# Performance work log

Measured on AMD Instinct MI355X. Metric: run time of the kernel, lower is better.

## Reference

```python
import jax, jax.numpy as jnp
import numpy as np

N = 50000      # nodes
E = 800000     # edges
B = 512        # graphs in batch
DRNL = 64      # drnl_dim (feature_dim = 0)
H = 256        # hidden


def setup_inputs() -> dict:
    key = jax.random.key(0)
    ks = jax.random.split(key, 12)
    x = jax.random.normal(ks[0], (N, DRNL), jnp.float32)
    edge_index = jax.random.randint(ks[1], (2, E), 0, N)
    batch_vec = jnp.sort(jax.random.randint(ks[2], (N,), 0, B))
    u_idx = jax.random.randint(ks[3], (B,), 0, N)
    v_idx = jax.random.randint(ks[4], (B,), 0, N)

    def glorot(k, shp):
        scale = jnp.sqrt(2.0 / (shp[0] + shp[1]))
        return (jax.random.normal(k, shp, jnp.float32) * scale).astype(jnp.float32)

    W0 = glorot(ks[5], (DRNL, H)); b0 = jnp.zeros((H,), jnp.float32)
    W1 = glorot(ks[6], (H, H));    b1 = jnp.zeros((H,), jnp.float32)
    W2 = glorot(ks[7], (H, H));    b2 = jnp.zeros((H,), jnp.float32)
    Wm1 = glorot(ks[8], (3 * H, H)); bm1 = jnp.zeros((H,), jnp.float32)
    Wm2 = glorot(ks[9], (H, 1));     bm2 = jnp.zeros((1,), jnp.float32)
    return dict(x=x, edge_index=edge_index, batch_vec=batch_vec,
                u_idx=u_idx, v_idx=v_idx,
                W0=W0, b0=b0, W1=W1, b1=b1, W2=W2, b2=b2,
                Wm1=Wm1, bm1=bm1, Wm2=Wm2, bm2=bm2)


def _gcn_encode(x, src, dst, Ws, bs):
    # Standard GCN: h' = D^-1/2 (A + I) D^-1/2 h W + b, ReLU between layers.
    n = x.shape[0]
    loop = jnp.arange(n)
    src2 = jnp.concatenate([src, loop])  # add self-loops
    dst2 = jnp.concatenate([dst, loop])
    deg = jax.ops.segment_sum(jnp.ones_like(dst2, x.dtype), dst2, num_segments=n)
    dis = jax.lax.rsqrt(jnp.maximum(deg, 1.0))          # D^-1/2
    norm = dis[src2] * dis[dst2]                         # per-edge norm [E+N]

    h = x
    for i, (W, b) in enumerate(zip(Ws, bs)):
        msg = h[src2] * norm[:, None]                    # gather + scale
        agg = jax.ops.segment_sum(msg, dst2, num_segments=n)
        h = agg @ W + b
        if i < len(Ws) - 1:
            h = jax.nn.relu(h)
    return h


def reference(x, edge_index, batch_vec, u_idx, v_idx,
              W0, b0, W1, b1, W2, b2, Wm1, bm1, Wm2, bm2):
    src, dst = edge_index[0], edge_index[1]
    h = _gcn_encode(x, src, dst, (W0, W1, W2), (b0, b1, b2))   # [N, H]

    # global_mean_pool over batch_vec -> [B, H]
    cnt = jax.ops.segment_sum(jnp.ones((h.shape[0],), h.dtype), batch_vec,
                              num_segments=B)
    g = jax.ops.segment_sum(h, batch_vec, num_segments=B) / \
        jnp.maximum(cnt, 1.0)[:, None]

    # concat [g, h[u], h[v]] -> MLP -> [B] logits
    z = jnp.concatenate([g, h[u_idx], h[v_idx]], axis=1)       # [B, 3H]
    z = jax.nn.relu(z @ Wm1 + bm1)
    return (z @ Wm2 + bm2).squeeze(-1)
```

## Files before the change

kernel.cpp:

```cpp
#include <hip/hip_runtime.h>
#include <hip/hip_bf16.h>
#include <stdint.h>

#ifndef DRNL
#define DRNL 64
#define HDIM 256
#endif

#define CHUNK 4096
#define BCAP 3072
#define SCAP 1536

typedef __attribute__((ext_vector_type(4))) float f32x4;
typedef __attribute__((ext_vector_type(8))) _Float16 f16x8;

__device__ __forceinline__ void async16(void* lds, const void* g) {
    __builtin_amdgcn_global_load_lds(
        (const __attribute__((address_space(1))) void*)g,
        (__attribute__((address_space(3))) void*)(char*)lds, 16, 0, 0);
}

__device__ __forceinline__ int imin(int a, int b) { return a < b ? a : b; }

__global__ __launch_bounds__(256) void k_misc(
    const int* __restrict__ batch,
    const float* __restrict__ x,
    const float* __restrict__ W0, const float* __restrict__ W1,
    const float* __restrict__ W2,
    int* __restrict__ gstart,
    _Float16* __restrict__ x16,
    _Float16* __restrict__ W0t, _Float16* __restrict__ W1t,
    _Float16* __restrict__ W2t,
    const int* __restrict__ dst, int* __restrict__ ghist,
    int E, int P, int SH, int NBUCK,
    int N, int B) {
    const int tid = threadIdx.x;

    if (blockIdx.x < P) {
        __shared__ int h[512];
        int p = blockIdx.x;
        for (int i = tid; i < NBUCK; i += 256) h[i] = 0;
        __syncthreads();
        int e0 = p * CHUNK, e1 = imin(e0 + CHUNK, E);
        for (int e = e0 + tid; e < e1; e += 256)
            atomicAdd(&h[dst[e] >> SH], 1);
        __syncthreads();
        for (int b = tid; b < NBUCK; b += 256)
            ghist[(size_t)b * P + p] = h[b];
        return;
    }

    const int bid  = blockIdx.x - P;
    const int gsz  = (gridDim.x - P) * 256;
    const int gid0 = bid * 256 + tid;

    for (int i = gid0; i < (DRNL + 2 * HDIM) * 256; i += gsz) {
        int b = i >> 8, c = i & 255;
        const float* W; _Float16* T; int k, K;
        if (b < DRNL)            { W = W0; T = W0t; k = b;              K = DRNL; }
        else if (b < DRNL + 256) { W = W1; T = W1t; k = b - DRNL;       K = HDIM; }
        else                     { W = W2; T = W2t; k = b - DRNL - 256; K = HDIM; }
        int KT = K >> 5;
        int cg = c >> 6, ct = (c >> 4) & 3, cl = c & 15;
        int kt = k >> 5, qq = (k >> 3) & 3, j = k & 7;
        int lane = (qq << 4) | cl;
        T[(((size_t)(cg * KT + kt) * 4 + ct) * 64 + lane) * 8 + j] =
            (_Float16)W[(size_t)k * 256 + c];
    }

    {
        const float4* x4 = (const float4*)x;
        f16x8* xv = (f16x8*)x16;
        int tot = N * DRNL / 8;
        for (int i = gid0; i < tot; i += gsz) {
            float4 a = x4[2 * i], b2 = x4[2 * i + 1];
            f16x8 o;
            o[0] = (_Float16)a.x;  o[1] = (_Float16)a.y;
            o[2] = (_Float16)a.z;  o[3] = (_Float16)a.w;
            o[4] = (_Float16)b2.x; o[5] = (_Float16)b2.y;
            o[6] = (_Float16)b2.z; o[7] = (_Float16)b2.w;
            xv[i] = o;
        }
    }

    for (int i = gid0; i <= N; i += gsz) {
        if (i == 0) {
            int b0 = batch[0];
            for (int b = 0; b <= b0; ++b) gstart[b] = 0;
        } else if (i == N) {
            int bl = batch[N - 1];
            for (int b = bl + 1; b <= B; ++b) gstart[b] = N;
        } else {
            int bp = batch[i - 1], bc = batch[i];
            if (bc != bp)
                for (int b = bp + 1; b <= bc; ++b) gstart[b] = i;
        }
    }
}

__global__ __launch_bounds__(256) void k_gbase(int* __restrict__ ghist,
                                               int* __restrict__ btot, int P) {
    __shared__ int s[256];
    int b = blockIdx.x, tid = threadIdx.x;
    int* row = ghist + (size_t)b * P;
    int carry = 0;
    for (int base = 0; base < P; base += 256) {
        int idx = base + tid;
        int v = (idx < P) ? row[idx] : 0;
        s[tid] = v;
        __syncthreads();
        for (int o = 1; o < 256; o <<= 1) {
            int t = (tid >= o) ? s[tid - o] : 0;
            __syncthreads();
            s[tid] += t;
            __syncthreads();
        }
        if (idx < P) row[idx] = carry + s[tid] - v;
        carry += s[255];
        __syncthreads();
    }
    if (tid == 0) btot[b] = carry;
}

__global__ __launch_bounds__(256) void k_btscan(const int* __restrict__ btot,
                                                int* __restrict__ bbase,
                                                int* __restrict__ rowptr,
                                                int NBUCK, int N, int E) {
    __shared__ int s[256];
    int tid = threadIdx.x;
    int carry = 0;
    for (int base = 0; base < NBUCK; base += 256) {
        int idx = base + tid;
        int v = (idx < NBUCK) ? btot[idx] : 0;
        s[tid] = v;
        __syncthreads();
        for (int o = 1; o < 256; o <<= 1) {
            int t = (tid >= o) ? s[tid - o] : 0;
            __syncthreads();
            s[tid] += t;
            __syncthreads();
        }
        if (idx < NBUCK) bbase[idx] = carry + s[tid] - v;
        carry += s[255];
        __syncthreads();
    }
    if (tid == 0) { bbase[NBUCK] = E; rowptr[N] = E; }
}

__global__ __launch_bounds__(256) void k_scatter(const int* __restrict__ src,
                                                 const int* __restrict__ dst,
                                                 const int* __restrict__ ghist,
                                                 const int* __restrict__ bbase,
                                                 int* __restrict__ tmp,
                                                 int E, int P, int SH, int NBUCK) {
    __shared__ int base[512];
    int p = blockIdx.x, tid = threadIdx.x;
    for (int b = tid; b < NBUCK; b += 256)
        base[b] = bbase[b] + ghist[(size_t)b * P + p];
    __syncthreads();
    int e0 = p * CHUNK, e1 = imin(e0 + CHUNK, E);
    int msk = (1 << SH) - 1;
    for (int e = e0 + tid; e < e1; e += 256) {
        int d = dst[e];
        int r = atomicAdd(&base[d >> SH], 1);
        tmp[r] = (src[e] << SH) | (d & msk);
    }
}

__global__ __launch_bounds__(256) void k_bsort(const int* __restrict__ tmp,
                                               const int* __restrict__ bbase,
                                               int* __restrict__ col,
                                               int* __restrict__ rowptr,
                                               float* __restrict__ dis,
                                               _Float16* __restrict__ x16,
                                               int SH, int N) {
    __shared__ int cnt[512];
    __shared__ int off[512];
    __shared__ int sscan[256];
    __shared__ int eL[BCAP];
    __shared__ unsigned short rnk[BCAP];
    __shared__ int sL[BCAP];
    int b = blockIdx.x, tid = threadIdx.x;
    int nodes = 1 << SH, node0 = b << SH, msk = nodes - 1;
    int lo = bbase[b], hi = bbase[b + 1], m = hi - lo;
    bool fast = (m <= BCAP);

    for (int i = tid; i < nodes; i += 256) cnt[i] = 0;
    __syncthreads();
    if (fast) {
        for (int i = tid; i < m; i += 256) {
            int v = tmp[lo + i];
            eL[i] = v;
            rnk[i] = (unsigned short)atomicAdd(&cnt[v & msk], 1);
        }
    } else {
        for (int i = tid; i < m; i += 256)
            atomicAdd(&cnt[tmp[lo + i] & msk], 1);
    }
    __syncthreads();
    int carry = 0;
    for (int base = 0; base < nodes; base += 256) {
        int idx = base + tid;
        int v = (idx < nodes) ? cnt[idx] : 0;
        sscan[tid] = v;
        __syncthreads();
        for (int o = 1; o < 256; o <<= 1) {
            int t = (tid >= o) ? sscan[tid - o] : 0;
            __syncthreads();
            sscan[tid] += t;
            __syncthreads();
        }
        if (idx < nodes) off[idx] = carry + sscan[tid] - v;
        carry += sscan[255];
        __syncthreads();
    }
    for (int i = tid; i < nodes; i += 256) {
        int node = node0 + i;
        if (node < N) {
            rowptr[node] = lo + off[i];
            dis[node]    = rsqrtf((float)cnt[i] + 1.f);
        }
    }
    int rlim = imin(nodes, N - node0);
    for (int u = tid; u < rlim * 8; u += 256) {
        int r = u >> 3, c = u & 7;
        float d = rsqrtf((float)cnt[r] + 1.f);
        f16x8* xv = (f16x8*)(x16 + (size_t)(node0 + r) * 64);
        f16x8 v = xv[c];
        f16x8 o;
#pragma unroll
        for (int k = 0; k < 8; ++k) o[k] = (_Float16)((float)v[k] * d);
        xv[c] = o;
    }
    __syncthreads();
    if (fast) {
        for (int i = tid; i < m; i += 256) {
            int v = eL[i];
            sL[off[v & msk] + rnk[i]] = v >> SH;
        }
        __syncthreads();
        for (int i = tid; i < m; i += 256) col[lo + i] = sL[i];
    } else {
        for (int i = tid; i < nodes; i += 256) cnt[i] = 0;
        __syncthreads();
        for (int i = tid; i < m; i += 256) {
            int v = tmp[lo + i];
            int d = v & msk;
            int r = atomicAdd(&cnt[d], 1);
            col[lo + off[d] + r] = v >> SH;
        }
    }
}

template <int FBLK>
__global__ __launch_bounds__(256) void k_agg(const _Float16* __restrict__ hs,
                                             const float* __restrict__ dis,
                                             const int* __restrict__ rowptr,
                                             const int* __restrict__ col,
                                             _Float16* __restrict__ A16, int N) {
    __shared__ int scol[SCAP];
    int node_wg, f;
    if constexpr (FBLK == 4) {
        int wg = blockIdx.x;
        int xcd = wg & 7;
        f = xcd >> 1;
        int half = xcd & 1;
        int NH = gridDim.x >> 3;
        node_wg = half * NH + (wg >> 3);
    } else {
        node_wg = blockIdx.x;
        f = 0;
    }
    const int n0 = imin(node_wg * 32, N);
    const int n1 = imin(node_wg * 32 + 32, N);
    const int e_lo = rowptr[n0];
    const int cnt = rowptr[n1] - e_lo;
    const bool useLds = (cnt <= SCAP);
    if (useLds)
        for (int i = threadIdx.x; i < cnt; i += 256) scol[i] = col[e_lo + i];
    __syncthreads();

    int lane = threadIdx.x & 63;
    int wv = threadIdx.x >> 6;
    int oct = lane >> 3;
    int fl = lane & 7;
    int gw = node_wg * 32 + wv * 8 + oct;
    bool valid = gw < N;
    int gwc = valid ? gw : N - 1;
    const size_t boff = (size_t)f * ((size_t)N * 64);
    const f16x8* hv = (const f16x8*)(hs + boff);
    float acc[8];
#pragma unroll
    for (int k = 0; k < 8; ++k) acc[k] = 0.f;

    int e0 = rowptr[gwc];
    int e1 = valid ? rowptr[gwc + 1] : e0;

    if (useLds) {
        int j  = e0 - e_lo;
        int eN = valid ? e1 - e_lo : j;
        while (__any(j < eN)) {
            bool a0 = j < eN, a1 = j + 1 < eN, a2 = j + 2 < eN, a3 = j + 3 < eN;
            int s0 = scol[a0 ? j : 0];
            int s1 = scol[a1 ? j + 1 : 0];
            int s2 = scol[a2 ? j + 2 : 0];
            int s3 = scol[a3 ? j + 3 : 0];
            float m0 = a0 ? 1.f : 0.f, m1 = a1 ? 1.f : 0.f;
            float m2 = a2 ? 1.f : 0.f, m3 = a3 ? 1.f : 0.f;
            f16x8 v0 = hv[(size_t)s0 * 8 + fl];
            f16x8 v1 = hv[(size_t)s1 * 8 + fl];
            f16x8 v2 = hv[(size_t)s2 * 8 + fl];
            f16x8 v3 = hv[(size_t)s3 * 8 + fl];
#pragma unroll
            for (int k = 0; k < 8; ++k) acc[k] += m0 * (float)v0[k];
#pragma unroll
            for (int k = 0; k < 8; ++k) acc[k] += m1 * (float)v1[k];
#pragma unroll
            for (int k = 0; k < 8; ++k) acc[k] += m2 * (float)v2[k];
#pragma unroll
            for (int k = 0; k < 8; ++k) acc[k] += m3 * (float)v3[k];
            j += 4;
        }
    } else {
        int j = e0;
        while (__any(j < e1)) {
            bool a0 = j < e1, a1 = j + 1 < e1, a2 = j + 2 < e1, a3 = j + 3 < e1;
            int s0 = col[a0 ? j : 0];
            int s1 = col[a1 ? j + 1 : 0];
            int s2 = col[a2 ? j + 2 : 0];
            int s3 = col[a3 ? j + 3 : 0];
            float m0 = a0 ? 1.f : 0.f, m1 = a1 ? 1.f : 0.f;
            float m2 = a2 ? 1.f : 0.f, m3 = a3 ? 1.f : 0.f;
            f16x8 v0 = hv[(size_t)s0 * 8 + fl];
            f16x8 v1 = hv[(size_t)s1 * 8 + fl];
            f16x8 v2 = hv[(size_t)s2 * 8 + fl];
            f16x8 v3 = hv[(size_t)s3 * 8 + fl];
#pragma unroll
            for (int k = 0; k < 8; ++k) acc[k] += m0 * (float)v0[k];
#pragma unroll
            for (int k = 0; k < 8; ++k) acc[k] += m1 * (float)v1[k];
#pragma unroll
            for (int k = 0; k < 8; ++k) acc[k] += m2 * (float)v2[k];
#pragma unroll
            for (int k = 0; k < 8; ++k) acc[k] += m3 * (float)v3[k];
            j += 4;
        }
    }

    float dn = dis[gwc];
    f16x8 hsv = hv[(size_t)gwc * 8 + fl];
    f16x8 o;
#pragma unroll
    for (int k = 0; k < 8; ++k)
        o[k] = (_Float16)((acc[k] + (float)hsv[k]) * dn);
    if (valid)
        __builtin_nontemporal_store(
            o, (f16x8*)(A16 + boff + (size_t)gw * 64 + fl * 8));
}

template <int K, int OUT_RELU, int SCALE>
__global__ __launch_bounds__(256, 1) void k_wgemm(const _Float16* __restrict__ A,
                                                  const _Float16* __restrict__ Wf,
                                                  const float* __restrict__ bias,
                                                  const float* __restrict__ dis,
                                                  _Float16* __restrict__ outh, int n) {
    constexpr int KT  = K / 32;
    constexpr int NFB = K / 64;
    constexpr int NI  = NFB * 2;
    constexpr int STG = NFB * 1024;
    __shared__ _Float16 sAll[4 * (STG + 1024)];

    const int tid  = threadIdx.x;
    const int lane = tid & 63;
    const int wv   = tid >> 6;
    const int c15  = lane & 15;
    const int q    = lane >> 4;
    const int row0 = blockIdx.x * 64;
    const size_t bstride = (size_t)n * 64;
    _Float16* sbuf = sAll + wv * (STG + 1024);
    _Float16* sO   = sbuf + STG;
    _Float16* ob   = outh + (size_t)wv * bstride;

    f16x8 wf[4][KT];
    const _Float16* wp = Wf + ((size_t)wv * KT * 4 * 64 + lane) * 8;
#pragma unroll
    for (int kt = 0; kt < KT; ++kt)
#pragma unroll
        for (int ct = 0; ct < 4; ++ct)
            wf[ct][kt] = *(const f16x8*)(wp + (size_t)((kt * 4 + ct) * 64) * 8);

    float bvl = bias[(wv << 6) + lane];
    float bv[4];
#pragma unroll
    for (int ct = 0; ct < 4; ++ct) bv[ct] = __shfl(bvl, (ct << 4) + c15);

    float dsv[4][4];
    if (SCALE) {
        float dvl = dis[imin(row0 + lane, n - 1)];
#pragma unroll
        for (int st = 0; st < 4; ++st)
#pragma unroll
            for (int r = 0; r < 4; ++r)
                dsv[st][r] = __shfl(dvl, (st << 4) + (q << 2) + r);
    }

#pragma unroll
    for (int st = 0; st < 4; ++st) {
        const int r0 = row0 + (st << 4);
#pragma unroll
        for (int i = 0; i < NI; ++i) {
            int s   = (i << 6) + lane;
            int fb  = s >> 7;
            int row = (s >> 3) & 15;
            int ch  = (s & 7) ^ (row & 7);
            int gr  = imin(r0 + row, n - 1);
            async16(sbuf + (size_t)s * 8,
                    A + (size_t)fb * bstride + (size_t)gr * 64 + ch * 8);
        }
        asm volatile("s_waitcnt vmcnt(0)" ::: "memory");
        __builtin_amdgcn_sched_barrier(0);

        f16x8 af[KT];
#pragma unroll
        for (int kt = 0; kt < KT; ++kt) {
            int off = (kt >> 1) * 1024 + c15 * 64 +
                      ((((kt & 1) * 4 + q) ^ (c15 & 7)) * 8);
            af[kt] = *(const f16x8*)(sbuf + off);
        }

        f32x4 acc[4];
#pragma unroll
        for (int ct = 0; ct < 4; ++ct) acc[ct] = (f32x4)0.f;
#pragma unroll
        for (int kt = 0; kt < KT; ++kt)
#pragma unroll
            for (int ct = 0; ct < 4; ++ct)
                acc[ct] = __builtin_amdgcn_mfma_f32_16x16x32_f16(
                    af[kt], wf[ct][kt], acc[ct], 0, 0, 0);

#pragma unroll
        for (int ct = 0; ct < 4; ++ct) {
#pragma unroll
            for (int r = 0; r < 4; ++r) {
                float v = acc[ct][r] + bv[ct];
                if (OUT_RELU) v = fmaxf(v, 0.f);
                if (SCALE) v *= dsv[st][r];
                int row = (q << 2) + r;
                int colx = (ct << 4) + c15;
                int sw = (((colx >> 3) ^ (row & 7)) << 3) | (colx & 7);
                sO[row * 64 + sw] = (_Float16)v;
            }
        }
#pragma unroll
        for (int ps = 0; ps < 2; ++ps) {
            int u = (ps << 6) + lane;
            int rr = u >> 3, ch2 = u & 7;
            f16x8 vv = *(const f16x8*)(sO + rr * 64 + ((ch2 ^ (rr & 7)) << 3));
            if (r0 + rr < n)
                *(f16x8*)(ob + (size_t)(r0 + rr) * 64 + ch2 * 8) = vv;
        }
    }
}

__global__ __launch_bounds__(256) void k_head(const _Float16* __restrict__ h,
                                              const int* __restrict__ gstart,
                                              const int* __restrict__ u,
                                              const int* __restrict__ v,
                                              const float* __restrict__ Wm1,
                                              const float* __restrict__ bm1,
                                              const float* __restrict__ Wm2,
                                              const float* __restrict__ bm2,
                                              float* __restrict__ out, int N) {
    int b = blockIdx.x;
    int t = threadIdx.x;
    __shared__ float z[3 * HDIM];
    __shared__ float red[4];
    const _Float16* hb = h + (size_t)(t >> 6) * ((size_t)N * 64) + (t & 63);
    int s = gstart[b], e = gstart[b + 1];
    float pa = 0.f;
    int i = s;
    for (; i + 3 < e; i += 4) {
        float a0 = (float)hb[(size_t)i * 64];
        float a1 = (float)hb[(size_t)(i + 1) * 64];
        float a2 = (float)hb[(size_t)(i + 2) * 64];
        float a3 = (float)hb[(size_t)(i + 3) * 64];
        pa += (a0 + a1) + (a2 + a3);
    }
    for (; i < e; ++i) pa += (float)hb[(size_t)i * 64];
    z[t]            = pa / fmaxf((float)(e - s), 1.f);
    z[HDIM + t]     = (float)hb[(size_t)u[b] * 64];
    z[2 * HDIM + t] = (float)hb[(size_t)v[b] * 64];
    __syncthreads();
    float acc[8];
#pragma unroll
    for (int k = 0; k < 8; ++k) acc[k] = 0.f;
    for (int k = 0; k < 3 * HDIM; k += 8) {
#pragma unroll
        for (int jj = 0; jj < 8; ++jj)
            acc[jj] = fmaf(z[k + jj], Wm1[(size_t)(k + jj) * HDIM + t], acc[jj]);
    }
    float sum = (((acc[0] + acc[1]) + (acc[2] + acc[3])) +
                 ((acc[4] + acc[5]) + (acc[6] + acc[7]))) + bm1[t];
    float hid = fmaxf(sum, 0.f);
    float p = hid * Wm2[t];
    for (int off = 32; off; off >>= 1) p += __shfl_down(p, off);
    if ((t & 63) == 0) red[t >> 6] = p;
    __syncthreads();
    if (t == 0) out[b] = red[0] + red[1] + red[2] + red[3] + bm2[0];
}

extern "C" void kernel_launch(void* const* d_in, const int* in_sizes, int n_in,
                              void* d_out, int out_size, void* d_ws, size_t ws_size,
                              hipStream_t stream) {
    const float* x    = (const float*)d_in[0];
    const int*   ei   = (const int*)d_in[1];
    const int*   batc = (const int*)d_in[2];
    const int*   uidx = (const int*)d_in[3];
    const int*   vidx = (const int*)d_in[4];
    const float* W0   = (const float*)d_in[5];
    const float* b0   = (const float*)d_in[6];
    const float* W1   = (const float*)d_in[7];
    const float* b1   = (const float*)d_in[8];
    const float* W2   = (const float*)d_in[9];
    const float* b2   = (const float*)d_in[10];
    const float* Wm1  = (const float*)d_in[11];
    const float* bm1  = (const float*)d_in[12];
    const float* Wm2  = (const float*)d_in[13];
    const float* bm2  = (const float*)d_in[14];
    float* out = (float*)d_out;

    const int N = in_sizes[0] / DRNL;
    const int E = in_sizes[1] / 2;
    const int B = in_sizes[3];
    const int* src = ei;
    const int* dst = ei + E;

    int SH = 7;
    while (((N + (1 << SH) - 1) >> SH) > 512) ++SH;
    const int NBUCK = (N + (1 << SH) - 1) >> SH;
    const int P = (E + CHUNK - 1) / CHUNK;

    char* w = (char*)d_ws;
    size_t off = 0;
    auto carve = [&](size_t bytes) {
        void* p = w + off;
        off = (off + bytes + 255) & ~(size_t)255;
        return p;
    };
    int*       rowptr = (int*)carve((size_t)(N + 1) * 4);
    int*       colA   = (int*)carve((size_t)E * 4);
    float*     dis    = (float*)carve((size_t)N * 4);
    int*       gstart = (int*)carve((size_t)(B + 1) * 4);
    _Float16*  A16    = (_Float16*)carve((size_t)N * HDIM * 2);
    _Float16*  h16    = (_Float16*)carve((size_t)N * HDIM * 2);
    _Float16*  x16    = (_Float16*)carve((size_t)N * DRNL * 2);
    _Float16*  W0t    = (_Float16*)carve((size_t)DRNL * HDIM * 2);
    _Float16*  W1t    = (_Float16*)carve((size_t)HDIM * HDIM * 2);
    _Float16*  W2t    = (_Float16*)carve((size_t)HDIM * HDIM * 2);
    int*       ghist  = (int*)carve((size_t)NBUCK * P * 4);
    int*       btot   = (int*)carve(512 * 4);
    int*       bbase  = (int*)carve(513 * 4);
    int*       tmpE   = (int*)carve((size_t)E * 4);
    (void)ws_size;

    k_misc<<<P + 1024, 256, 0, stream>>>(batc, x, W0, W1, W2, gstart,
                                         x16, W0t, W1t, W2t,
                                         dst, ghist, E, P, SH, NBUCK, N, B);
    k_gbase<<<NBUCK, 256, 0, stream>>>(ghist, btot, P);
    k_btscan<<<1, 256, 0, stream>>>(btot, bbase, rowptr, NBUCK, N, E);
    k_scatter<<<P, 256, 0, stream>>>(src, dst, ghist, bbase, tmpE, E, P, SH, NBUCK);
    k_bsort<<<NBUCK, 256, 0, stream>>>(tmpE, bbase, colA, rowptr, dis, x16, SH, N);

    int gemmb = (N + 63) / 64;
    int NB = (N + 31) / 32;
    int NH = (NB + 1) / 2;
    int aggb4 = 8 * NH;

    k_agg<1><<<NB, 256, 0, stream>>>(x16, dis, rowptr, colA, A16, N);
    k_wgemm<DRNL, 1, 1><<<gemmb, 256, 0, stream>>>(A16, W0t, b0, dis, h16, N);
    k_agg<4><<<aggb4, 256, 0, stream>>>(h16, dis, rowptr, colA, A16, N);
    k_wgemm<HDIM, 1, 1><<<gemmb, 256, 0, stream>>>(A16, W1t, b1, dis, h16, N);
    k_agg<4><<<aggb4, 256, 0, stream>>>(h16, dis, rowptr, colA, A16, N);
    k_wgemm<HDIM, 0, 0><<<gemmb, 256, 0, stream>>>(A16, W2t, b2, dis, h16, N);

    k_head<<<B, 256, 0, stream>>>(h16, gstart, uidx, vidx, Wm1, bm1, Wm2, bm2, out, N);
}
```

Baseline: 286.3 us.

## Degree-sort nodes within buckets for aggregation and double-buffer GEMM A staging

The bucket sort now builds a per-bucket permutation that orders nodes by in-degree (capped at 63). The aggregation kernels walk nodes through this permutation, so the 8 nodes sharing a wave have similar edge counts, which reduces divergence and idle lanes. To make that work, each aggregation block stages the whole bucket's column list into LDS, and the LDS capacity is doubled to hold it. Separately, the weight GEMM now double-buffers its A-tile async loads so the next 16-row stage is fetched while the current one runs on MFMA. The costs are more LDS per block and an extra indirection for every node lookup; the larger stage also makes the LDS fallback path more likely.

```diff
diff --git a/kernel.cpp b/kernel.cpp
--- a/kernel.cpp
+++ b/kernel.cpp
@@ -9,7 +9,7 @@
 
 #define CHUNK 4096
 #define BCAP 3072
-#define SCAP 1536
+#define SCAP 3072
 
 typedef __attribute__((ext_vector_type(4))) float f32x4;
 typedef __attribute__((ext_vector_type(8))) _Float16 f16x8;
@@ -173,10 +173,13 @@
                                                int* __restrict__ rowptr,
                                                float* __restrict__ dis,
                                                _Float16* __restrict__ x16,
+                                               int* __restrict__ perm,
                                                int SH, int N) {
     __shared__ int cnt[512];
     __shared__ int off[512];
     __shared__ int sscan[256];
+    __shared__ int dh[64];
+    __shared__ int dbs[64];
     __shared__ int eL[BCAP];
     __shared__ unsigned short rnk[BCAP];
     __shared__ int sL[BCAP];
@@ -186,6 +189,7 @@
     bool fast = (m <= BCAP);
 
     for (int i = tid; i < nodes; i += 256) cnt[i] = 0;
+    for (int i = tid; i < 64; i += 256) dh[i] = 0;
     __syncthreads();
     if (fast) {
         for (int i = tid; i < m; i += 256) {
@@ -214,6 +218,7 @@
         carry += sscan[255];
         __syncthreads();
     }
+    int rlim = imin(nodes, N - node0);
     for (int i = tid; i < nodes; i += 256) {
         int node = node0 + i;
         if (node < N) {
@@ -221,7 +226,21 @@
             dis[node]    = rsqrtf((float)cnt[i] + 1.f);
         }
     }
-    int rlim = imin(nodes, N - node0);
+    for (int i = tid; i < rlim; i += 256)
+        atomicAdd(&dh[imin(cnt[i], 63)], 1);
+    __syncthreads();
+    if (tid == 0) {
+        int c = 0;
+        for (int d = 0; d < 64; ++d) { int t = dh[d]; dbs[d] = c; c += t; }
+    }
+    __syncthreads();
+    for (int i = tid; i < 64; i += 256) dh[i] = 0;
+    __syncthreads();
+    for (int i = tid; i < rlim; i += 256) {
+        int d = imin(cnt[i], 63);
+        int r = dbs[d] + atomicAdd(&dh[d], 1);
+        perm[node0 + r] = node0 + i;
+    }
     for (int u = tid; u < rlim * 8; u += 256) {
         int r = u >> 3, c = u & 7;
         float d = rsqrtf((float)cnt[r] + 1.f);
@@ -257,7 +276,9 @@
                                              const float* __restrict__ dis,
                                              const int* __restrict__ rowptr,
                                              const int* __restrict__ col,
-                                             _Float16* __restrict__ A16, int N) {
+                                             const int* __restrict__ perm,
+                                             _Float16* __restrict__ A16,
+                                             int N, int SH) {
     __shared__ int scol[SCAP];
     int node_wg, f;
     if constexpr (FBLK == 4) {
@@ -271,30 +292,32 @@
         node_wg = blockIdx.x;
         f = 0;
     }
-    const int n0 = imin(node_wg * 32, N);
-    const int n1 = imin(node_wg * 32 + 32, N);
-    const int e_lo = rowptr[n0];
-    const int cnt = rowptr[n1] - e_lo;
-    const bool useLds = (cnt <= SCAP);
+    if (node_wg * 32 >= N) return;
+    const int buck = (node_wg * 32) >> SH;
+    const int b_lo = buck << SH;
+    const int b_hi = imin(b_lo + (1 << SH), N);
+    const int e_lo = rowptr[b_lo];
+    const int cntE = rowptr[b_hi] - e_lo;
+    const bool useLds = (cntE <= SCAP);
     if (useLds)
-        for (int i = threadIdx.x; i < cnt; i += 256) scol[i] = col[e_lo + i];
+        for (int i = threadIdx.x; i < cntE; i += 256) scol[i] = col[e_lo + i];
     __syncthreads();
 
     int lane = threadIdx.x & 63;
     int wv = threadIdx.x >> 6;
     int oct = lane >> 3;
     int fl = lane & 7;
-    int gw = node_wg * 32 + wv * 8 + oct;
-    bool valid = gw < N;
-    int gwc = valid ? gw : N - 1;
+    int slot = node_wg * 32 + wv * 8 + oct;
+    bool valid = slot < N;
+    int gw = valid ? perm[slot] : 0;
     const size_t boff = (size_t)f * ((size_t)N * 64);
     const f16x8* hv = (const f16x8*)(hs + boff);
     float acc[8];
 #pragma unroll
     for (int k = 0; k < 8; ++k) acc[k] = 0.f;
 
-    int e0 = rowptr[gwc];
-    int e1 = valid ? rowptr[gwc + 1] : e0;
+    int e0 = rowptr[gw];
+    int e1 = valid ? rowptr[gw + 1] : e0;
 
     if (useLds) {
         int j  = e0 - e_lo;
@@ -347,8 +370,8 @@
         }
     }
 
-    float dn = dis[gwc];
-    f16x8 hsv = hv[(size_t)gwc * 8 + fl];
+    float dn = dis[gw];
+    f16x8 hsv = hv[(size_t)gw * 8 + fl];
     f16x8 o;
 #pragma unroll
     for (int k = 0; k < 8; ++k)
@@ -368,7 +391,7 @@
     constexpr int NFB = K / 64;
     constexpr int NI  = NFB * 2;
     constexpr int STG = NFB * 1024;
-    __shared__ _Float16 sAll[4 * (STG + 1024)];
+    __shared__ _Float16 sAll[4 * (2 * STG + 1024)];
 
     const int tid  = threadIdx.x;
     const int lane = tid & 63;
@@ -377,35 +400,12 @@
     const int q    = lane >> 4;
     const int row0 = blockIdx.x * 64;
     const size_t bstride = (size_t)n * 64;
-    _Float16* sbuf = sAll + wv * (STG + 1024);
-    _Float16* sO   = sbuf + STG;
-    _Float16* ob   = outh + (size_t)wv * bstride;
-
-    f16x8 wf[4][KT];
-    const _Float16* wp = Wf + ((size_t)wv * KT * 4 * 64 + lane) * 8;
-#pragma unroll
-    for (int kt = 0; kt < KT; ++kt)
-#pragma unroll
-        for (int ct = 0; ct < 4; ++ct)
-            wf[ct][kt] = *(const f16x8*)(wp + (size_t)((kt * 4 + ct) * 64) * 8);
-
-    float bvl = bias[(wv << 6) + lane];
-    float bv[4];
-#pragma unroll
-    for (int ct = 0; ct < 4; ++ct) bv[ct] = __shfl(bvl, (ct << 4) + c15);
-
-    float dsv[4][4];
-    if (SCALE) {
-        float dvl = dis[imin(row0 + lane, n - 1)];
-#pragma unroll
-        for (int st = 0; st < 4; ++st)
-#pragma unroll
-            for (int r = 0; r < 4; ++r)
-                dsv[st][r] = __shfl(dvl, (st << 4) + (q << 2) + r);
-    }
-
-#pragma unroll
-    for (int st = 0; st < 4; ++st) {
+    _Float16* sbufA = sAll + wv * (2 * STG + 1024);
+    _Float16* sbufB = sbufA + STG;
+    _Float16* sO    = sbufA + 2 * STG;
+    _Float16* ob    = outh + (size_t)wv * bstride;
+
+    auto stage = [&](_Float16* dstp, int st) {
         const int r0 = row0 + (st << 4);
 #pragma unroll
         for (int i = 0; i < NI; ++i) {
@@ -414,18 +414,56 @@
             int row = (s >> 3) & 15;
             int ch  = (s & 7) ^ (row & 7);
             int gr  = imin(r0 + row, n - 1);
-            async16(sbuf + (size_t)s * 8,
+            async16(dstp + (size_t)s * 8,
                     A + (size_t)fb * bstride + (size_t)gr * 64 + ch * 8);
         }
-        asm volatile("s_waitcnt vmcnt(0)" ::: "memory");
+    };
+
+    stage(sbufA, 0);
+
+    f16x8 wf[4][KT];
+    const _Float16* wp = Wf + ((size_t)wv * KT * 4 * 64 + lane) * 8;
+#pragma unroll
+    for (int kt = 0; kt < KT; ++kt)
+#pragma unroll
+        for (int ct = 0; ct < 4; ++ct)
+            wf[ct][kt] = *(const f16x8*)(wp + (size_t)((kt * 4 + ct) * 64) * 8);
+
+    float bvl = bias[(wv << 6) + lane];
+    float bv[4];
+#pragma unroll
+    for (int ct = 0; ct < 4; ++ct) bv[ct] = __shfl(bvl, (ct << 4) + c15);
+
+    float dsv[4][4];
+    if (SCALE) {
+        float dvl = dis[imin(row0 + lane, n - 1)];
+#pragma unroll
+        for (int st = 0; st < 4; ++st)
+#pragma unroll
+            for (int r = 0; r < 4; ++r)
+                dsv[st][r] = __shfl(dvl, (st << 4) + (q << 2) + r);
+    }
+
+#pragma unroll
+    for (int st = 0; st < 4; ++st) {
+        if (st < 3) stage((st & 1) ? sbufA : sbufB, st + 1);
+        if (st < 3) {
+            if constexpr (NI == 8)
+                asm volatile("s_waitcnt vmcnt(8)" ::: "memory");
+            else
+                asm volatile("s_waitcnt vmcnt(2)" ::: "memory");
+        } else {
+            asm volatile("s_waitcnt vmcnt(2)" ::: "memory");
+        }
         __builtin_amdgcn_sched_barrier(0);
 
+        const _Float16* buf = (st & 1) ? sbufB : sbufA;
         f16x8 af[KT];
 #pragma unroll
         for (int kt = 0; kt < KT; ++kt) {
             int off = (kt >> 1) * 1024 + c15 * 64 +
                       ((((kt & 1) * 4 + q) ^ (c15 & 7)) * 8);
-            af[kt] = *(const f16x8*)(sbuf + off);
+            af[kt] = *(const f16x8*)(buf + off);
         }
 
         f32x4 acc[4];
@@ -438,6 +476,7 @@
                 acc[ct] = __builtin_amdgcn_mfma_f32_16x16x32_f16(
                     af[kt], wf[ct][kt], acc[ct], 0, 0, 0);
 
+        const int r0 = row0 + (st << 4);
 #pragma unroll
         for (int ct = 0; ct < 4; ++ct) {
 #pragma unroll
@@ -551,6 +590,7 @@
     int*       colA   = (int*)carve((size_t)E * 4);
     float*     dis    = (float*)carve((size_t)N * 4);
     int*       gstart = (int*)carve((size_t)(B + 1) * 4);
+    int*       perm   = (int*)carve((size_t)N * 4);
     _Float16*  A16    = (_Float16*)carve((size_t)N * HDIM * 2);
     _Float16*  h16    = (_Float16*)carve((size_t)N * HDIM * 2);
     _Float16*  x16    = (_Float16*)carve((size_t)N * DRNL * 2);
@@ -569,18 +609,19 @@
     k_gbase<<<NBUCK, 256, 0, stream>>>(ghist, btot, P);
     k_btscan<<<1, 256, 0, stream>>>(btot, bbase, rowptr, NBUCK, N, E);
     k_scatter<<<P, 256, 0, stream>>>(src, dst, ghist, bbase, tmpE, E, P, SH, NBUCK);
-    k_bsort<<<NBUCK, 256, 0, stream>>>(tmpE, bbase, colA, rowptr, dis, x16, SH, N);
+    k_bsort<<<NBUCK, 256, 0, stream>>>(tmpE, bbase, colA, rowptr, dis, x16,
+                                       perm, SH, N);
 
     int gemmb = (N + 63) / 64;
     int NB = (N + 31) / 32;
     int NH = (NB + 1) / 2;
     int aggb4 = 8 * NH;
 
-    k_agg<1><<<NB, 256, 0, stream>>>(x16, dis, rowptr, colA, A16, N);
+    k_agg<1><<<NB, 256, 0, stream>>>(x16, dis, rowptr, colA, perm, A16, N, SH);
     k_wgemm<DRNL, 1, 1><<<gemmb, 256, 0, stream>>>(A16, W0t, b0, dis, h16, N);
-    k_agg<4><<<aggb4, 256, 0, stream>>>(h16, dis, rowptr, colA, A16, N);
+    k_agg<4><<<aggb4, 256, 0, stream>>>(h16, dis, rowptr, colA, perm, A16, N, SH);
     k_wgemm<HDIM, 1, 1><<<gemmb, 256, 0, stream>>>(A16, W1t, b1, dis, h16, N);
-    k_agg<4><<<aggb4, 256, 0, stream>>>(h16, dis, rowptr, colA, A16, N);
+    k_agg<4><<<aggb4, 256, 0, stream>>>(h16, dis, rowptr, colA, perm, A16, N, SH);
     k_wgemm<HDIM, 0, 0><<<gemmb, 256, 0, stream>>>(A16, W2t, b2, dis, h16, N);
 
     k_head<<<B, 256, 0, stream>>>(h16, gstart, uidx, vidx, Wm1, bm1, Wm2, bm2, out, N);
```

Result: slower. 296.4 us (+3.5%).

## Fuse layer-0 aggregation with its weight GEMM into one kernel

Applied to the files above, without the earlier changes.

Replaces the separate layer-0 aggregation kernel and the K=64 GEMM kernel with one fused kernel. Each workgroup aggregates 64 rows of neighbour features into LDS, then multiplies them by W0 using MFMA, with weights held in registers, and applies bias, ReLU and degree scaling. The A16 intermediate no longer makes a round trip through global memory and one launch is removed. In exchange, each workgroup runs the gather and the GEMM serially, uses fewer workgroups than the old 32-node aggregation grid, and needs more LDS.

```diff
diff --git a/kernel.cpp b/kernel.cpp
--- a/kernel.cpp
+++ b/kernel.cpp
@@ -10,6 +10,7 @@
 #define CHUNK 4096
 #define BCAP 3072
 #define SCAP 1536
+#define SCAP0 2048
 
 typedef __attribute__((ext_vector_type(4))) float f32x4;
 typedef __attribute__((ext_vector_type(8))) _Float16 f16x8;
@@ -252,25 +253,185 @@
     }
 }
 
-template <int FBLK>
-__global__ __launch_bounds__(256) void k_agg(const _Float16* __restrict__ hs,
-                                             const float* __restrict__ dis,
-                                             const int* __restrict__ rowptr,
-                                             const int* __restrict__ col,
-                                             _Float16* __restrict__ A16, int N) {
+__global__ __launch_bounds__(256) void k_l0(
+    const _Float16* __restrict__ hs, const float* __restrict__ dis,
+    const int* __restrict__ rowptr, const int* __restrict__ col,
+    const _Float16* __restrict__ Wf, const float* __restrict__ bias,
+    _Float16* __restrict__ outh, int n) {
+    constexpr int KT = 2;
+    __shared__ _Float16 sA[64 * 64];
+    __shared__ int scol[SCAP0];
+    __shared__ _Float16 sOut[4 * 16 * 64];
+
+    const int tid  = threadIdx.x;
+    const int lane = tid & 63;
+    const int wv   = tid >> 6;
+    const int c15  = lane & 15;
+    const int q    = lane >> 4;
+    const int row0 = blockIdx.x * 64;
+    const size_t bstride = (size_t)n * 64;
+    _Float16* sO = sOut + wv * (16 * 64);
+    _Float16* ob = outh + (size_t)wv * bstride;
+
+    f16x8 wf[4][KT];
+    const _Float16* wp = Wf + ((size_t)wv * KT * 4 * 64 + lane) * 8;
+#pragma unroll
+    for (int kt = 0; kt < KT; ++kt)
+#pragma unroll
+        for (int ct = 0; ct < 4; ++ct)
+            wf[ct][kt] = *(const f16x8*)(wp + (size_t)((kt * 4 + ct) * 64) * 8);
+    float bvl = bias[(wv << 6) + lane];
+    float bv[4];
+#pragma unroll
+    for (int ct = 0; ct < 4; ++ct) bv[ct] = __shfl(bvl, (ct << 4) + c15);
+    float dvl = dis[imin(row0 + lane, n - 1)];
+    float dsv[4][4];
+#pragma unroll
+    for (int st = 0; st < 4; ++st)
+#pragma unroll
+        for (int r = 0; r < 4; ++r)
+            dsv[st][r] = __shfl(dvl, (st << 4) + (q << 2) + r);
+
+    const int n1 = imin(row0 + 64, n);
+    const int e_lo = rowptr[row0];
+    const int cntE = rowptr[n1] - e_lo;
+    const bool useLds = (cntE <= SCAP0);
+    if (useLds)
+        for (int i = tid; i < cntE; i += 256) scol[i] = col[e_lo + i];
+    __syncthreads();
+
+    const f16x8* hv = (const f16x8*)hs;
+    const int fl = lane & 7;
+#pragma unroll
+    for (int ps = 0; ps < 2; ++ps) {
+        int loc = ps * 32 + (tid >> 3);
+        int gw = row0 + loc;
+        bool valid = gw < n;
+        int gwc = valid ? gw : n - 1;
+        float acc[8];
+#pragma unroll
+        for (int k = 0; k < 8; ++k) acc[k] = 0.f;
+        int e0 = rowptr[gwc];
+        int e1 = valid ? rowptr[gwc + 1] : e0;
+        if (useLds) {
+            int j  = e0 - e_lo;
+            int eN = valid ? e1 - e_lo : j;
+            while (__any(j < eN)) {
+                bool a0 = j < eN, a1 = j + 1 < eN, a2 = j + 2 < eN, a3 = j + 3 < eN;
+                int s0 = scol[a0 ? j : 0];
+                int s1 = scol[a1 ? j + 1 : 0];
+                int s2 = scol[a2 ? j + 2 : 0];
+                int s3 = scol[a3 ? j + 3 : 0];
+                float m0 = a0 ? 1.f : 0.f, m1 = a1 ? 1.f : 0.f;
+                float m2 = a2 ? 1.f : 0.f, m3 = a3 ? 1.f : 0.f;
+                f16x8 v0 = hv[(size_t)s0 * 8 + fl];
+                f16x8 v1 = hv[(size_t)s1 * 8 + fl];
+                f16x8 v2 = hv[(size_t)s2 * 8 + fl];
+                f16x8 v3 = hv[(size_t)s3 * 8 + fl];
+#pragma unroll
+                for (int k = 0; k < 8; ++k) acc[k] += m0 * (float)v0[k];
+#pragma unroll
+                for (int k = 0; k < 8; ++k) acc[k] += m1 * (float)v1[k];
+#pragma unroll
+                for (int k = 0; k < 8; ++k) acc[k] += m2 * (float)v2[k];
+#pragma unroll
+                for (int k = 0; k < 8; ++k) acc[k] += m3 * (float)v3[k];
+                j += 4;
+            }
+        } else {
+            int j = e0;
+            while (__any(j < e1)) {
+                bool a0 = j < e1, a1 = j + 1 < e1, a2 = j + 2 < e1, a3 = j + 3 < e1;
+                int s0 = col[a0 ? j : 0];
+                int s1 = col[a1 ? j + 1 : 0];
+                int s2 = col[a2 ? j + 2 : 0];
+                int s3 = col[a3 ? j + 3 : 0];
+                float m0 = a0 ? 1.f : 0.f, m1 = a1 ? 1.f : 0.f;
+                float m2 = a2 ? 1.f : 0.f, m3 = a3 ? 1.f : 0.f;
+                f16x8 v0 = hv[(size_t)s0 * 8 + fl];
+                f16x8 v1 = hv[(size_t)s1 * 8 + fl];
+                f16x8 v2 = hv[(size_t)s2 * 8 + fl];
+                f16x8 v3 = hv[(size_t)s3 * 8 + fl];
+#pragma unroll
+                for (int k = 0; k < 8; ++k) acc[k] += m0 * (float)v0[k];
+#pragma unroll
+                for (int k = 0; k < 8; ++k) acc[k] += m1 * (float)v1[k];
+#pragma unroll
+                for (int k = 0; k < 8; ++k) acc[k] += m2 * (float)v2[k];
+#pragma unroll
+                for (int k = 0; k < 8; ++k) acc[k] += m3 * (float)v3[k];
+                j += 4;
+            }
+        }
+        f16x8 o;
+        if (valid) {
+            float dn = dis[gwc];
+            f16x8 hsv = hv[(size_t)gwc * 8 + fl];
+#pragma unroll
+            for (int k = 0; k < 8; ++k)
+                o[k] = (_Float16)((acc[k] + (float)hsv[k]) * dn);
+        } else {
+#pragma unroll
+            for (int k = 0; k < 8; ++k) o[k] = (_Float16)0.f;
+        }
+        *(f16x8*)(sA + loc * 64 + ((fl ^ (loc & 7)) << 3)) = o;
+    }
+    __syncthreads();
+
+#pragma unroll
+    for (int st = 0; st < 4; ++st) {
+        const int r0   = row0 + (st << 4);
+        const int rowl = (st << 4) + c15;
+        f16x8 af[KT];
+#pragma unroll
+        for (int kt = 0; kt < KT; ++kt)
+            af[kt] = *(const f16x8*)(sA + rowl * 64 +
+                                     (((kt * 4 + q) ^ (c15 & 7)) << 3));
+        f32x4 acc2[4];
+#pragma unroll
+        for (int ct = 0; ct < 4; ++ct) acc2[ct] = (f32x4)0.f;
+#pragma unroll
+        for (int kt = 0; kt < KT; ++kt)
+#pragma unroll
+            for (int ct = 0; ct < 4; ++ct)
+                acc2[ct] = __builtin_amdgcn_mfma_f32_16x16x32_f16(
+                    af[kt], wf[ct][kt], acc2[ct], 0, 0, 0);
+#pragma unroll
+        for (int ct = 0; ct < 4; ++ct) {
+#pragma unroll
+            for (int r = 0; r < 4; ++r) {
+                float v = acc2[ct][r] + bv[ct];
+                v = fmaxf(v, 0.f);
+                v *= dsv[st][r];
+                int row = (q << 2) + r;
+                int colx = (ct << 4) + c15;
+                int sw = (((colx >> 3) ^ (row & 7)) << 3) | (colx & 7);
+                sO[row * 64 + sw] = (_Float16)v;
+            }
+        }
+#pragma unroll
+        for (int pp = 0; pp < 2; ++pp) {
+            int u = (pp << 6) + lane;
+            int rr = u >> 3, ch2 = u & 7;
+            f16x8 vv = *(const f16x8*)(sO + rr * 64 + ((ch2 ^ (rr & 7)) << 3));
+            if (r0 + rr < n)
+                *(f16x8*)(ob + (size_t)(r0 + rr) * 64 + ch2 * 8) = vv;
+        }
+    }
+}
+
+__global__ __launch_bounds__(256) void k_agg4(const _Float16* __restrict__ hs,
+                                              const float* __restrict__ dis,
+                                              const int* __restrict__ rowptr,
+                                              const int* __restrict__ col,
+                                              _Float16* __restrict__ A16, int N) {
     __shared__ int scol[SCAP];
-    int node_wg, f;
-    if constexpr (FBLK == 4) {
-        int wg = blockIdx.x;
-        int xcd = wg & 7;
-        f = xcd >> 1;
-        int half = xcd & 1;
-        int NH = gridDim.x >> 3;
-        node_wg = half * NH + (wg >> 3);
-    } else {
-        node_wg = blockIdx.x;
-        f = 0;
-    }
+    int wg = blockIdx.x;
+    int xcd = wg & 7;
+    int f = xcd >> 1;
+    int half = xcd & 1;
+    int NH = gridDim.x >> 3;
+    int node_wg = half * NH + (wg >> 3);
     const int n0 = imin(node_wg * 32, N);
     const int n1 = imin(node_wg * 32 + 32, N);
     const int e_lo = rowptr[n0];
@@ -576,11 +737,10 @@
     int NH = (NB + 1) / 2;
     int aggb4 = 8 * NH;
 
-    k_agg<1><<<NB, 256, 0, stream>>>(x16, dis, rowptr, colA, A16, N);
-    k_wgemm<DRNL, 1, 1><<<gemmb, 256, 0, stream>>>(A16, W0t, b0, dis, h16, N);
-    k_agg<4><<<aggb4, 256, 0, stream>>>(h16, dis, rowptr, colA, A16, N);
+    k_l0<<<gemmb, 256, 0, stream>>>(x16, dis, rowptr, colA, W0t, b0, h16, N);
+    k_agg4<<<aggb4, 256, 0, stream>>>(h16, dis, rowptr, colA, A16, N);
     k_wgemm<HDIM, 1, 1><<<gemmb, 256, 0, stream>>>(A16, W1t, b1, dis, h16, N);
-    k_agg<4><<<aggb4, 256, 0, stream>>>(h16, dis, rowptr, colA, A16, N);
+    k_agg4<<<aggb4, 256, 0, stream>>>(h16, dis, rowptr, colA, A16, N);
     k_wgemm<HDIM, 0, 0><<<gemmb, 256, 0, stream>>>(A16, W2t, b2, dis, h16, N);
 
     k_head<<<B, 256, 0, stream>>>(h16, gstart, uidx, vidx, Wm1, bm1, Wm2, bm2, out, N);
```

Result: no change. 290.4 us (+1.4%).
